# Performance work log

Measured on AMD Instinct MI355X. Metric: run time of the kernel, lower is better.

Reference implementation:

```python
import jax, jax.numpy as jnp
import numpy as np

B, S, D = 2, 2048, 1024
FFN = 4096
E, TOPK = 4, 2
H, WIN = 8, 128
EPS = 1e-6


def rmsnorm(x, w):
    rms = jax.lax.rsqrt(jnp.mean(x * x, axis=-1, keepdims=True) + EPS)
    return x * rms * w


def linear_scan(x, a):
    """h_t = a_t * h_{t-1} + x_t along axis=1, via associative scan."""
    def comb(c1, c2):
        a1, x1 = c1
        a2, x2 = c2
        return (a1 * a2, a2 * x1 + x2)
    _, h = jax.lax.associative_scan(comb, (a, x), axis=1)
    return h


def mingru_expert(xn, Wg, bg, Wv, bv, Wd, bd):
    g = xn @ Wg + bg
    v = xn @ Wv + bv
    d = xn @ Wd + bd
    x_scan = jax.nn.sigmoid(g) * jnp.tanh(v)
    a = 0.001 + 0.998 * jax.nn.sigmoid(d)
    return linear_scan(x_scan, a)


def setup_inputs() -> dict:
    key = jax.random.key(0)
    ks = jax.random.split(key, 16)
    sc = 0.02
    return {
        "x": jax.random.normal(ks[0], (B, S, D), jnp.float32),
        "rms_mix_w": jnp.ones((D,), jnp.float32),
        "gate_w": jax.random.normal(ks[1], (D, E), jnp.float32) * sc,
        "Wg": jax.random.normal(ks[2], (E, D, D), jnp.float32) * sc,
        "bg": jnp.zeros((E, D), jnp.float32),
        "Wv": jax.random.normal(ks[3], (E, D, D), jnp.float32) * sc,
        "bv": jnp.zeros((E, D), jnp.float32),
        "Wd": jax.random.normal(ks[4], (E, D, D), jnp.float32) * sc,
        "bd": jnp.ones((E, D), jnp.float32),  # decay_bias_init = 1.0
        "rms_attn_w": jnp.ones((D,), jnp.float32),
        "w_qkv": jax.random.normal(ks[5], (D, 3 * D), jnp.float32) * sc,
        "w_attn_out": jax.random.normal(ks[6], (D, D), jnp.float32) * sc,
        "rms_ffn_w": jnp.ones((D,), jnp.float32),
        "w_ffn_gate": jax.random.normal(ks[7], (D, FFN), jnp.float32) * sc,
        "w_ffn_up": jax.random.normal(ks[8], (D, FFN), jnp.float32) * sc,
        "w_ffn_out": jax.random.normal(ks[9], (FFN, D), jnp.float32) * sc,
    }


def reference(x, rms_mix_w, gate_w, Wg, bg, Wv, bv, Wd, bd,
              rms_attn_w, w_qkv, w_attn_out,
              rms_ffn_w, w_ffn_gate, w_ffn_up, w_ffn_out):
    # --- MoE-MinGRU mixer -------------------------------------------------
    xn = rmsnorm(x, rms_mix_w)
    gate_logits = xn @ gate_w                         # [B,S,E]
    top_vals, top_idx = jax.lax.top_k(gate_logits, TOPK)
    weights = jax.nn.softmax(top_vals, axis=-1)       # [B,S,K]
    expert_outs = jax.vmap(mingru_expert, in_axes=(None, 0, 0, 0, 0, 0, 0))(
        xn, Wg, bg, Wv, bv, Wd, bd)                   # [E,B,S,D]
    expert_outs = jnp.moveaxis(expert_outs, 0, 2)     # [B,S,E,D]
    gathered = jnp.take_along_axis(expert_outs, top_idx[..., None], axis=2)  # [B,S,K,D]
    mix = jnp.sum(weights[..., None] * gathered, axis=2)
    x = x + mix

    # --- Sliding-window causal attention ----------------------------------
    xn = rmsnorm(x, rms_attn_w)
    dh = D // H
    qkv = (xn @ w_qkv).reshape(B, S, 3, H, dh)
    q, k, v = qkv[:, :, 0], qkv[:, :, 1], qkv[:, :, 2]  # [B,S,H,dh]
    scores = jnp.einsum("bqhd,bkhd->bhqk", q, k) / jnp.sqrt(jnp.float32(dh))
    i = jnp.arange(S)[:, None]
    j = jnp.arange(S)[None, :]
    allowed = (j <= i) & (j > i - WIN)
    scores = jnp.where(allowed, scores, -jnp.inf)
    attn = jax.nn.softmax(scores, axis=-1)
    ao = jnp.einsum("bhqk,bkhd->bqhd", attn, v).reshape(B, S, D)
    x = x + ao @ w_attn_out

    # --- SwiGLU FFN --------------------------------------------------------
    xn = rmsnorm(x, rms_ffn_w)
    ffn = (jax.nn.silu(xn @ w_ffn_gate) * (xn @ w_ffn_up)) @ w_ffn_out
    return x + ffn
```

## Files before the change

kernel.cpp:

```cpp
#include <hip/hip_runtime.h>
#include <hip/hip_bf16.h>
#include <math.h>

constexpr int kB   = 2;
constexpr int kS   = 2048;
constexpr int kD   = 1024;
constexpr int kFFN = 4096;
constexpr int kM   = kB * kS;
constexpr int kH   = 8;
constexpr int kDH  = 128;
constexpr int kNC  = 64;
constexpr int kT   = kS / kNC;
constexpr int kNE  = 12288;

typedef unsigned short u16;
typedef __attribute__((ext_vector_type(8))) short short8;
typedef __attribute__((ext_vector_type(4))) float f32x4;

__device__ __forceinline__ float sigf(float x) { return 1.0f / (1.0f + __expf(-x)); }
__device__ __forceinline__ float bu2f(u16 u) { return __uint_as_float(((unsigned)u) << 16); }
__device__ __forceinline__ u16 f2bu(float f) {
    __hip_bfloat16 h = __float2bfloat16(f);
    return reinterpret_cast<u16&>(h);
}
__device__ __forceinline__ void async16(const void* g, void* l) {
    __builtin_amdgcn_global_load_lds((const __attribute__((address_space(1))) void*)g,
                                     (__attribute__((address_space(3))) void*)l, 16, 0, 0);
}
__device__ __forceinline__ int xcd_swz(int orig, int nwg) {
    const int xcd = orig & 7;
    const int q8 = nwg >> 3, r8 = nwg & 7;
    return (xcd < r8 ? xcd * (q8 + 1) : r8 * (q8 + 1) + (xcd - r8) * q8) + (orig >> 3);
}

__global__ __launch_bounds__(256) void rmsnorm_k(const float* __restrict__ x,
                                                 const float* __restrict__ w,
                                                 u16* __restrict__ o)
{
    __shared__ float red[4];
    const int row = blockIdx.x;
    const int t = threadIdx.x;
    float4 v = ((const float4*)(x + (size_t)row * kD))[t];
    float ss = v.x*v.x + v.y*v.y + v.z*v.z + v.w*v.w;
    #pragma unroll
    for (int m = 32; m; m >>= 1) ss += __shfl_xor(ss, m);
    if ((t & 63) == 0) red[t >> 6] = ss;
    __syncthreads();
    float tot = red[0] + red[1] + red[2] + red[3];
    float r = rsqrtf(tot * (1.0f / (float)kD) + 1e-6f);
    float4 wv = ((const float4*)w)[t];
    ushort4 u;
    u.x = f2bu(v.x * r * wv.x); u.y = f2bu(v.y * r * wv.y);
    u.z = f2bu(v.z * r * wv.z); u.w = f2bu(v.w * r * wv.w);
    ((ushort4*)(o + (size_t)row * kD))[t] = u;
}

__global__ __launch_bounds__(64) void routing_k(const float* __restrict__ x,
                                                const float* __restrict__ wmix,
                                                const float* __restrict__ gw,
                                                float* __restrict__ wts,
                                                int* __restrict__ idx)
{
    const int row = blockIdx.x;
    const int lane = threadIdx.x;
    const float* xr = x + (size_t)row * kD;
    float ss = 0.0f;
    for (int d = lane; d < kD; d += 64) { float v = xr[d]; ss = fmaf(v, v, ss); }
    #pragma unroll
    for (int m = 32; m; m >>= 1) ss += __shfl_xor(ss, m);
    float r = rsqrtf(ss * (1.0f / (float)kD) + 1e-6f);

    float a0 = 0, a1 = 0, a2 = 0, a3 = 0;
    for (int d = lane; d < kD; d += 64) {
        float xv = xr[d] * wmix[d];
        float4 g = ((const float4*)gw)[d];
        a0 = fmaf(xv, g.x, a0);
        a1 = fmaf(xv, g.y, a1);
        a2 = fmaf(xv, g.z, a2);
        a3 = fmaf(xv, g.w, a3);
    }
    #pragma unroll
    for (int m = 32; m; m >>= 1) {
        a0 += __shfl_xor(a0, m);
        a1 += __shfl_xor(a1, m);
        a2 += __shfl_xor(a2, m);
        a3 += __shfl_xor(a3, m);
    }
    if (lane == 0) {
        float a[4] = {a0, a1, a2, a3};
        int i0 = 0; float v0 = a[0];
        #pragma unroll
        for (int e = 1; e < 4; ++e) if (a[e] > v0) { v0 = a[e]; i0 = e; }
        int i1 = -1; float v1 = -INFINITY;
        #pragma unroll
        for (int e = 0; e < 4; ++e) if (e != i0 && a[e] > v1) { v1 = a[e]; i1 = e; }
        float e1 = __expf(r * (v1 - v0));
        float dn = 1.0f + e1;
        wts[row * 2 + 0] = 1.0f / dn;
        wts[row * 2 + 1] = e1 / dn;
        idx[row * 2 + 0] = i0;
        idx[row * 2 + 1] = i1;
    }
}

__global__ __launch_bounds__(256) void transp_k(const float* __restrict__ src,
                                                u16* __restrict__ dst,
                                                int rows, int cols,
                                                size_t sstride, size_t dstride)
{
    __shared__ float t[32][33];
    const float* s = src + blockIdx.z * sstride;
    u16* d = dst + blockIdx.z * dstride;
    const int c0 = blockIdx.x * 32, r0 = blockIdx.y * 32;
    const int tc = threadIdx.x & 31, tr4 = (threadIdx.x >> 5) * 4;
    #pragma unroll
    for (int i = 0; i < 4; ++i)
        t[tr4 + i][tc] = s[(size_t)(r0 + tr4 + i) * cols + c0 + tc];
    __syncthreads();
    #pragma unroll
    for (int i = 0; i < 4; ++i) {
        int cc = tr4 + i;
        d[(size_t)(c0 + cc) * rows + r0 + tc] = f2bu(t[tc][cc]);
    }
}

__global__ __launch_bounds__(256) void biaspack_k(const float* __restrict__ bg,
                                                  const float* __restrict__ bv,
                                                  const float* __restrict__ bd,
                                                  float* __restrict__ pb)
{
    int e = blockIdx.y;
    int r = blockIdx.x * 256 + threadIdx.x;
    const float* src = (r < 1024) ? bg : (r < 2048) ? bv : bd;
    pb[e * 3072 + r] = src[e * 1024 + (r & 1023)];
}

template<bool BIAS, bool SILU, bool MUL>
__global__ __launch_bounds__(512, 2) void gemmA_k(
    const u16* __restrict__ A, const u16* __restrict__ BT,
    const float* __restrict__ bias, const u16* __restrict__ mulsrc,
    u16* __restrict__ Cout, int N, int K)
{
    __shared__ __align__(16) u16 lds[2][32768];
    const int tid = threadIdx.x;
    const int l = tid & 63;
    const int w = tid >> 6;
    const int wr = w >> 2, wc = w & 3;
    const int fr = l & 15, g = l >> 4;

    const int gx = gridDim.x;
    const int wg = xcd_swz(blockIdx.y * gx + blockIdx.x, gx * gridDim.y);
    const int bm = (wg / gx) * 256, bn = (wg % gx) * 256;

    const int srow = l >> 3;
    const int scol = (l & 7) ^ srow;
    const u16* gA = A  + (size_t)(bm + srow) * K + scol * 8;
    const u16* gB = BT + (size_t)(bn + srow) * K + scol * 8;

    auto STAGE = [&](int kt, int sb) {
        u16* dst = lds[sb] + l * 8;
        const int k0 = kt * 64;
        #pragma unroll
        for (int i = 0; i < 4; ++i) {
            int chunk = w * 4 + i;
            async16(gA + (size_t)chunk * 8 * K + k0, dst + chunk * 512);
            async16(gB + (size_t)chunk * 8 * K + k0, dst + 16384 + chunk * 512);
        }
    };

    f32x4 acc[8][4];
    #pragma unroll
    for (int m = 0; m < 8; ++m)
        #pragma unroll
        for (int n = 0; n < 4; ++n) acc[m][n] = (f32x4){0.f, 0.f, 0.f, 0.f};

    STAGE(0, 0);
    __syncthreads();
    const int nt = K >> 6;
    for (int t = 0; t < nt; ++t) {
        const int cb = t & 1;
        if (t + 1 < nt) STAGE(t + 1, cb ^ 1);
        const u16* bA = lds[cb];
        const u16* bB = lds[cb] + 16384;
        #pragma unroll
        for (int ks = 0; ks < 2; ++ks) {
            const int xo = ((ks * 4 + g) ^ (fr & 7)) * 8;
            short8 b[4];
            #pragma unroll
            for (int n = 0; n < 4; ++n)
                b[n] = *(const short8*)(bB + (wc * 64 + n * 16 + fr) * 64 + xo);
            #pragma unroll
            for (int m = 0; m < 8; ++m) {
                short8 a = *(const short8*)(bA + (wr * 128 + m * 16 + fr) * 64 + xo);
                #pragma unroll
                for (int n = 0; n < 4; ++n)
                    acc[m][n] = __builtin_amdgcn_mfma_f32_16x16x32_bf16(a, b[n], acc[m][n], 0, 0, 0);
            }
        }
        __syncthreads();
    }

    const int orow0 = bm + wr * 128 + g * 4;
    const int ocol0 = bn + wc * 64 + fr;
    float bi[4];
    if constexpr (BIAS) {
        #pragma unroll
        for (int n = 0; n < 4; ++n) bi[n] = bias[ocol0 + n * 16];
    }
    #pragma unroll
    for (int m = 0; m < 8; ++m) {
        #pragma unroll
        for (int r = 0; r < 4; ++r) {
            const size_t ro = (size_t)(orow0 + m * 16 + r) * N;
            #pragma unroll
            for (int n = 0; n < 4; ++n) {
                const size_t off = ro + ocol0 + n * 16;
                float v = acc[m][n][r];
                if constexpr (BIAS) v += bi[n];
                if constexpr (SILU) v = v * sigf(v);
                if constexpr (MUL)  v *= bu2f(mulsrc[off]);
                Cout[off] = f2bu(v);
            }
        }
    }
}

__global__ __launch_bounds__(256, 2) void gemmO_k(
    const u16* __restrict__ A, const u16* __restrict__ BT,
    const float* __restrict__ res, float* __restrict__ Cout,
    int N, int K)
{
    __shared__ __align__(16) u16 lds[3][20480];
    const int tid = threadIdx.x;
    const int l = tid & 63;
    const int w = tid >> 6;
    const int fr = l & 15, g = l >> 4;

    const int gx = gridDim.x;
    const int wg = xcd_swz(blockIdx.y * gx + blockIdx.x, gx * gridDim.y);
    const int bm = (wg / gx) * 256, bn = (wg % gx) * 64;

    const int srow = l >> 3;
    const int scol = (l & 7) ^ srow;
    const u16* gA = A  + (size_t)(bm + srow) * K + scol * 8;
    const u16* gB = BT + (size_t)(bn + srow) * K + scol * 8;

    auto STAGE = [&](int kt, int sb) {
        u16* dst = lds[sb] + l * 8;
        const int k0 = kt * 64;
        #pragma unroll
        for (int i = 0; i < 8; ++i) {
            int chunk = w * 8 + i;
            async16(gA + (size_t)chunk * 8 * K + k0, dst + chunk * 512);
        }
        #pragma unroll
        for (int i = 0; i < 2; ++i) {
            int chunk = w * 2 + i;
            async16(gB + (size_t)chunk * 8 * K + k0, dst + 16384 + chunk * 512);
        }
    };

    f32x4 acc[4][4];
    #pragma unroll
    for (int m = 0; m < 4; ++m)
        #pragma unroll
        for (int n = 0; n < 4; ++n) acc[m][n] = (f32x4){0.f, 0.f, 0.f, 0.f};

    STAGE(0, 0);
    STAGE(1, 1);
    const int nt = K >> 6;
    int cs = 0;
    for (int t = 0; t < nt; ++t) {
        if (t + 1 < nt) asm volatile("s_waitcnt vmcnt(10)" ::: "memory");
        else            asm volatile("s_waitcnt vmcnt(0)" ::: "memory");
        __builtin_amdgcn_s_barrier();
        __builtin_amdgcn_sched_barrier(0);
        if (t + 2 < nt) {
            int ns = cs + 2; if (ns >= 3) ns -= 3;
            STAGE(t + 2, ns);
        }
        const u16* bA = lds[cs];
        const u16* bB = lds[cs] + 16384;
        #pragma unroll
        for (int ks = 0; ks < 2; ++ks) {
            const int xo = ((ks * 4 + g) ^ (fr & 7)) * 8;
            short8 a[4], b[4];
            #pragma unroll
            for (int m = 0; m < 4; ++m)
                a[m] = *(const short8*)(bA + (w * 64 + m * 16 + fr) * 64 + xo);
            #pragma unroll
            for (int n = 0; n < 4; ++n)
                b[n] = *(const short8*)(bB + (n * 16 + fr) * 64 + xo);
            #pragma unroll
            for (int m = 0; m < 4; ++m)
                #pragma unroll
                for (int n = 0; n < 4; ++n)
                    acc[m][n] = __builtin_amdgcn_mfma_f32_16x16x32_bf16(a[m], b[n], acc[m][n], 0, 0, 0);
        }
        cs = (cs == 2) ? 0 : cs + 1;
    }

    const int orow0 = bm + w * 64 + g * 4;
    const int ocol0 = bn + fr;
    #pragma unroll
    for (int m = 0; m < 4; ++m) {
        #pragma unroll
        for (int r = 0; r < 4; ++r) {
            const size_t ro = (size_t)(orow0 + m * 16 + r) * N;
            #pragma unroll
            for (int n = 0; n < 4; ++n) {
                const size_t off = ro + ocol0 + n * 16;
                Cout[off] = acc[m][n][r] + res[off];
            }
        }
    }
}

__global__ __launch_bounds__(256) void scan1_k(const u16* __restrict__ gvdall,
                                               float* __restrict__ sumA,
                                               float* __restrict__ sumX)
{
    const int e = blockIdx.y;
    int i = blockIdx.x * 256 + threadIdx.x;
    int d = i & (kD - 1);
    int c = (i >> 10) & (kNC - 1);
    int b = i >> 16;
    const u16* gvd = gvdall + e * 3072;
    size_t base = ((size_t)b * kS + c * kT) * kNE + d;
    float A = 1.0f, X = 0.0f;
    for (int t = 0; t < kT; ++t) {
        size_t ix = base + (size_t)t * kNE;
        float xs = sigf(bu2f(gvd[ix])) * tanhf(bu2f(gvd[ix + 1024]));
        float a  = 0.001f + 0.998f * sigf(bu2f(gvd[ix + 2048]));
        A *= a;
        X = fmaf(a, X, xs);
    }
    size_t si = ((size_t)(e * kNC + c) * kB + b) * kD + d;
    sumA[si] = A;
    sumX[si] = X;
}

__global__ __launch_bounds__(256) void scan2_k(const float* __restrict__ sumA,
                                               const float* __restrict__ sumX,
                                               float* __restrict__ carry)
{
    const int e = blockIdx.y;
    int bd = blockIdx.x * 256 + threadIdx.x;
    float h = 0.0f;
    for (int c = 0; c < kNC; ++c) {
        size_t si = ((size_t)(e * kNC + c)) * (kB * kD) + bd;
        carry[si] = h;
        h = fmaf(sumA[si], h, sumX[si]);
    }
}

__global__ __launch_bounds__(256) void scan3_k(const u16* __restrict__ gvdall,
                                               const float* __restrict__ carry,
                                               const int* __restrict__ tidx,
                                               u16* __restrict__ slot0,
                                               u16* __restrict__ slot1)
{
    const int e = blockIdx.y;
    int i = blockIdx.x * 256 + threadIdx.x;
    int d = i & (kD - 1);
    int c = (i >> 10) & (kNC - 1);
    int b = i >> 16;
    const u16* gvd = gvdall + e * 3072;
    size_t base = ((size_t)b * kS + c * kT) * kNE + d;
    float h = carry[((size_t)(e * kNC + c) * kB + b) * kD + d];
    const int tok0 = b * kS + c * kT;
    for (int t = 0; t < kT; ++t) {
        size_t ix = base + (size_t)t * kNE;
        float xs = sigf(bu2f(gvd[ix])) * tanhf(bu2f(gvd[ix + 1024]));
        float a  = 0.001f + 0.998f * sigf(bu2f(gvd[ix + 2048]));
        h = fmaf(a, h, xs);
        const int tok = tok0 + t;
        const size_t o = (size_t)tok * kD + d;
        if (e == tidx[tok * 2])          slot0[o] = f2bu(h);
        else if (e == tidx[tok * 2 + 1]) slot1[o] = f2bu(h);
    }
}

__global__ __launch_bounds__(256) void mix_k(const float* __restrict__ x,
                                             const u16* __restrict__ slot0,
                                             const u16* __restrict__ slot1,
                                             const float* __restrict__ wts,
                                             float* __restrict__ xo)
{
    size_t i = (size_t)blockIdx.x * 256 + threadIdx.x;
    int m = (int)(i >> 8);
    float w0 = wts[m * 2 + 0], w1 = wts[m * 2 + 1];
    float4 xv = ((const float4*)x)[i];
    ushort4 h0 = ((const ushort4*)slot0)[i];
    ushort4 h1 = ((const ushort4*)slot1)[i];
    float4 o;
    o.x = xv.x + w0 * bu2f(h0.x) + w1 * bu2f(h1.x);
    o.y = xv.y + w0 * bu2f(h0.y) + w1 * bu2f(h1.y);
    o.z = xv.z + w0 * bu2f(h0.z) + w1 * bu2f(h1.z);
    o.w = xv.w + w0 * bu2f(h0.w) + w1 * bu2f(h1.w);
    ((float4*)xo)[i] = o;
}

__global__ __launch_bounds__(256) void transpV_k(const u16* __restrict__ qkvb,
                                                 u16* __restrict__ vT)
{
    __shared__ u16 t[64][68];
    const int tid = threadIdx.x;
    const int s0 = blockIdx.x * 64;
    const int d0 = blockIdx.y * 64;
    const int bh = blockIdx.z;
    const int bb = bh >> 3, hh = bh & 7;
    const u16* src = qkvb + (size_t)(bb * kS + s0) * 3072 + 2048 + hh * kDH + d0;
    for (int idx = tid; idx < 64 * 16; idx += 256) {
        int sl = idx >> 4, c4 = (idx & 15) * 4;
        *(ushort4*)&t[sl][c4] = *(const ushort4*)(src + (size_t)sl * 3072 + c4);
    }
    __syncthreads();
    u16* dst = vT + ((size_t)bh * kDH + d0) * kS + s0;
    for (int idx = tid; idx < 64 * 16; idx += 256) {
        int dl = idx >> 4, s4 = (idx & 15) * 4;
        ushort4 v;
        v.x = t[s4 + 0][dl]; v.y = t[s4 + 1][dl];
        v.z = t[s4 + 2][dl]; v.w = t[s4 + 3][dl];
        *(ushort4*)(dst + (size_t)dl * kS + s4) = v;
    }
}

__global__ __launch_bounds__(256) void attn_mfma_k(const u16* __restrict__ qkvb,
                                                   const u16* __restrict__ vT,
                                                   u16* __restrict__ aob)
{
    __shared__ __align__(16) u16 KV[26112];
    __shared__ __align__(16) u16 P[4 * 16 * 200];

    const int tid = threadIdx.x;
    const int lane = tid & 63;
    const int w = tid >> 6;
    const int fr = lane & 15, g = lane >> 4;
    const int q0 = blockIdx.x * 64;
    const int hh = blockIdx.y;
    const int bb = blockIdx.z;
    const int kbase = q0 - 128;
    const float scale = 0.08838834764831845f;

    const u16* qkv_b = qkvb + (size_t)bb * kS * 3072 + hh * kDH;

    for (int idx = tid; idx < 192 * 16; idx += 256) {
        int k = idx >> 4, c = idx & 15;
        int kg = kbase + k; if (kg < 0) kg = 0;
        short8 v = *(const short8*)(qkv_b + (size_t)kg * 3072 + 1024 + c * 8);
        *(short8*)(&KV[k * 136 + c * 8]) = v;
    }
    short8 qf[4];
    {
        const u16* qrow = qkv_b + (size_t)(q0 + w * 16 + fr) * 3072 + g * 8;
        #pragma unroll
        for (int s = 0; s < 4; ++s) qf[s] = *(const short8*)(qrow + s * 32);
    }
    __syncthreads();

    f32x4 sacc[12];
    #pragma unroll
    for (int f = 0; f < 12; ++f) sacc[f] = (f32x4){0.f, 0.f, 0.f, 0.f};
    #pragma unroll
    for (int s = 0; s < 4; ++s) {
        #pragma unroll
        for (int f = 0; f < 12; ++f) {
            short8 bfr = *(const short8*)(&KV[(f * 16 + fr) * 136 + s * 32 + g * 8]);
            sacc[f] = __builtin_amdgcn_mfma_f32_16x16x32_bf16(qf[s], bfr, sacc[f], 0, 0, 0);
        }
    }

    float p[12][4];
    #pragma unroll
    for (int r = 0; r < 4; ++r) {
        const int ql = w * 16 + g * 4 + r;
        int kmin = 128 - q0; if (kmin < ql + 1) kmin = ql + 1;
        const int kmax = ql + 128;
        float mx = -1e30f;
        #pragma unroll
        for (int f = 0; f < 12; ++f) {
            int kl = f * 16 + fr;
            float sv = (kl >= kmin && kl <= kmax) ? sacc[f][r] * scale : -1e30f;
            p[f][r] = sv;
            mx = fmaxf(mx, sv);
        }
        mx = fmaxf(mx, __shfl_xor(mx, 1));
        mx = fmaxf(mx, __shfl_xor(mx, 2));
        mx = fmaxf(mx, __shfl_xor(mx, 4));
        mx = fmaxf(mx, __shfl_xor(mx, 8));
        float l = 0.f;
        #pragma unroll
        for (int f = 0; f < 12; ++f) { float e = __expf(p[f][r] - mx); p[f][r] = e; l += e; }
        l += __shfl_xor(l, 1);
        l += __shfl_xor(l, 2);
        l += __shfl_xor(l, 4);
        l += __shfl_xor(l, 8);
        float linv = 1.0f / l;
        #pragma unroll
        for (int f = 0; f < 12; ++f) p[f][r] *= linv;
    }

    {
        u16* pw = &P[(w * 16) * 200];
        #pragma unroll
        for (int r = 0; r < 4; ++r)
            #pragma unroll
            for (int f = 0; f < 12; ++f)
                pw[(g * 4 + r) * 200 + f * 16 + fr] = f2bu(p[f][r]);
    }
    __syncthreads();

    {
        const u16* vrow = vT + (size_t)(bb * kH + hh) * kDH * kS;
        for (int idx = tid; idx < 128 * 25; idx += 256) {
            int d = idx / 25, c = idx % 25;
            if (c < 24) {
                int s0k = kbase + c * 8;
                short8 v;
                if (s0k < 0) v = (short8){0, 0, 0, 0, 0, 0, 0, 0};
                else v = *(const short8*)(vrow + (size_t)d * kS + s0k);
                *(short8*)(&KV[d * 200 + c * 8]) = v;
            }
        }
    }
    __syncthreads();

    f32x4 oacc[8];
    #pragma unroll
    for (int f = 0; f < 8; ++f) oacc[f] = (f32x4){0.f, 0.f, 0.f, 0.f};
    const u16* pr = &P[(w * 16 + fr) * 200 + g * 8];
    #pragma unroll
    for (int s = 0; s < 6; ++s) {
        short8 afr = *(const short8*)(pr + s * 32);
        #pragma unroll
        for (int f = 0; f < 8; ++f) {
            short8 bfr = *(const short8*)(&KV[(f * 16 + fr) * 200 + s * 32 + g * 8]);
            oacc[f] = __builtin_amdgcn_mfma_f32_16x16x32_bf16(afr, bfr, oacc[f], 0, 0, 0);
        }
    }
    u16* orow = aob + ((size_t)(bb * kS + q0 + w * 16 + g * 4) * kD) + hh * kDH + fr;
    #pragma unroll
    for (int r = 0; r < 4; ++r)
        #pragma unroll
        for (int f = 0; f < 8; ++f)
            orow[(size_t)r * kD + f * 16] = f2bu(oacc[f][r]);
}

extern "C" void kernel_launch(void* const* d_in, const int* in_sizes, int n_in,
                              void* d_out, int out_size, void* d_ws, size_t ws_size,
                              hipStream_t stream)
{
    (void)in_sizes; (void)n_in; (void)out_size; (void)ws_size;

    const float* x          = (const float*)d_in[0];
    const float* rms_mix    = (const float*)d_in[1];
    const float* gate_w     = (const float*)d_in[2];
    const float* Wg         = (const float*)d_in[3];
    const float* bg         = (const float*)d_in[4];
    const float* Wv         = (const float*)d_in[5];
    const float* bv         = (const float*)d_in[6];
    const float* Wd         = (const float*)d_in[7];
    const float* bd         = (const float*)d_in[8];
    const float* rms_attn   = (const float*)d_in[9];
    const float* w_qkv      = (const float*)d_in[10];
    const float* w_attn_out = (const float*)d_in[11];
    const float* rms_ffn    = (const float*)d_in[12];
    const float* w_ffn_gate = (const float*)d_in[13];
    const float* w_ffn_up   = (const float*)d_in[14];
    const float* w_ffn_out  = (const float*)d_in[15];
    float* out = (float*)d_out;

    const size_t MD = (size_t)kM * kD;
    const size_t M1 = 1024ull * 1024;
    char* p = (char*)d_ws;
    auto take = [&](size_t n) { char* r = p; p += (n + 255) & ~(size_t)255; return r; };

    u16*   xnb    = (u16*)take(MD * 2);
    u16*   gvdall = (u16*)take((size_t)kM * kNE * 2);
    u16*   qkvb   = gvdall;
    u16*   hidA   = gvdall;
    u16*   hidB   = gvdall + (size_t)kM * kFFN;
    u16*   ehb    = (u16*)take(4 * MD * 2);
    u16*   slot0  = ehb;
    u16*   slot1  = ehb + MD;
    u16*   aob    = ehb;
    u16*   vTb    = ehb + MD;
    u16*   wbuf   = (u16*)take(12ull * M1 * 2);
    float* pbias  = (float*)take((size_t)kNE * 4);
    float* sumA   = (float*)take(4ull * kNC * kB * kD * 4);
    float* sumX   = (float*)take(4ull * kNC * kB * kD * 4);
    float* carry  = (float*)take(4ull * kNC * kB * kD * 4);
    float* wts    = (float*)take((size_t)2 * kM * 4);
    int*   tidx   = (int*)take((size_t)2 * kM * 4);

    const dim3 blk(256);

    transp_k<<<dim3(32, 32, 4), blk, 0, stream>>>(Wg, wbuf, 1024, 1024,
                                                  (size_t)kD * kD, 3 * M1);
    transp_k<<<dim3(32, 32, 4), blk, 0, stream>>>(Wv, wbuf + M1, 1024, 1024,
                                                  (size_t)kD * kD, 3 * M1);
    transp_k<<<dim3(32, 32, 4), blk, 0, stream>>>(Wd, wbuf + 2 * M1, 1024, 1024,
                                                  (size_t)kD * kD, 3 * M1);
    biaspack_k<<<dim3(12, 4), blk, 0, stream>>>(bg, bv, bd, pbias);

    rmsnorm_k<<<kM, blk, 0, stream>>>(x, rms_mix, xnb);
    routing_k<<<kM, dim3(64), 0, stream>>>(x, rms_mix, gate_w, wts, tidx);

    gemmA_k<true, false, false><<<dim3(kNE / 256, kM / 256), dim3(512), 0, stream>>>(
        xnb, wbuf, pbias, nullptr, gvdall, kNE, 1024);
    const int scan_blocks = kB * kD * kNC / 256;
    scan1_k<<<dim3(scan_blocks, 4), blk, 0, stream>>>(gvdall, sumA, sumX);
    scan2_k<<<dim3(kB * kD / 256, 4), blk, 0, stream>>>(sumA, sumX, carry);
    scan3_k<<<dim3(scan_blocks, 4), blk, 0, stream>>>(gvdall, carry, tidx, slot0, slot1);

    mix_k<<<(int)(MD / 1024), blk, 0, stream>>>(x, slot0, slot1, wts, out);

    rmsnorm_k<<<kM, blk, 0, stream>>>(out, rms_attn, xnb);
    transp_k<<<dim3(96, 32, 1), blk, 0, stream>>>(w_qkv, wbuf, 1024, 3072, 0, 0);
    gemmA_k<false, false, false><<<dim3(3072 / 256, kM / 256), dim3(512), 0, stream>>>(
        xnb, wbuf, nullptr, nullptr, qkvb, 3072, 1024);
    transpV_k<<<dim3(kS / 64, 2, kB * kH), blk, 0, stream>>>(qkvb, vTb);
    attn_mfma_k<<<dim3(kS / 64, kH, kB), blk, 0, stream>>>(qkvb, vTb, aob);
    transp_k<<<dim3(32, 32, 1), blk, 0, stream>>>(w_attn_out, wbuf + 3 * M1, 1024, 1024, 0, 0);
    gemmO_k<<<dim3(1024 / 64, kM / 256), blk, 0, stream>>>(
        aob, wbuf + 3 * M1, out, out, 1024, 1024);

    rmsnorm_k<<<kM, blk, 0, stream>>>(out, rms_ffn, xnb);
    transp_k<<<dim3(128, 32, 1), blk, 0, stream>>>(w_ffn_gate, wbuf + 4 * M1, 1024, 4096, 0, 0);
    transp_k<<<dim3(128, 32, 1), blk, 0, stream>>>(w_ffn_up, wbuf + 8 * M1, 1024, 4096, 0, 0);
    transp_k<<<dim3(32, 128, 1), blk, 0, stream>>>(w_ffn_out, wbuf, 4096, 1024, 0, 0);
    gemmA_k<false, true, false><<<dim3(kFFN / 256, kM / 256), dim3(512), 0, stream>>>(
        xnb, wbuf + 4 * M1, nullptr, nullptr, hidA, kFFN, 1024);
    gemmA_k<false, false, true><<<dim3(kFFN / 256, kM / 256), dim3(512), 0, stream>>>(
        xnb, wbuf + 8 * M1, nullptr, hidA, hidB, kFFN, 1024);
    gemmO_k<<<dim3(1024 / 64, kM / 256), blk, 0, stream>>>(
        hidB, wbuf, out, out, 1024, 4096);
}
```

Baseline: 479.1 us.

## Rework output GEMM to 512-thread double-buffered tiles; nontemporal expert stores

The output-projection GEMM now uses 8 warps in a 4x2 arrangement, each computing a 64x32 sub-tile, with a simpler double-buffered LDS pipeline synchronized by __syncthreads instead of a triple-buffered vmcnt-based pipeline. This aims to raise parallelism per block and cut per-thread accumulator registers, at the cost of a shallower prefetch depth and full barriers each iteration. The large expert-projection GEMM also writes its bf16 output with nontemporal stores, to reduce cache pollution from a buffer that is streamed once by the scan kernels.

Measured after the change: 484.5 us (median of 3 runs). No clear change (+1.1%).

```diff
diff --git a/kernel.cpp b/kernel.cpp
--- a/kernel.cpp
+++ b/kernel.cpp
@@ -135,7 +135,7 @@
     pb[e * 3072 + r] = src[e * 1024 + (r & 1023)];
 }
 
-template<bool BIAS, bool SILU, bool MUL>
+template<bool BIAS, bool SILU, bool MUL, bool NT>
 __global__ __launch_bounds__(512, 2) void gemmA_k(
     const u16* __restrict__ A, const u16* __restrict__ BT,
     const float* __restrict__ bias, const u16* __restrict__ mulsrc,
@@ -219,21 +219,23 @@
                 if constexpr (BIAS) v += bi[n];
                 if constexpr (SILU) v = v * sigf(v);
                 if constexpr (MUL)  v *= bu2f(mulsrc[off]);
-                Cout[off] = f2bu(v);
+                if constexpr (NT) __builtin_nontemporal_store((short)f2bu(v), (short*)(Cout + off));
+                else              Cout[off] = f2bu(v);
             }
         }
     }
 }
 
-__global__ __launch_bounds__(256, 2) void gemmO_k(
+__global__ __launch_bounds__(512, 2) void gemmO_k(
     const u16* __restrict__ A, const u16* __restrict__ BT,
     const float* __restrict__ res, float* __restrict__ Cout,
     int N, int K)
 {
-    __shared__ __align__(16) u16 lds[3][20480];
+    __shared__ __align__(16) u16 lds[2][20480];
     const int tid = threadIdx.x;
     const int l = tid & 63;
     const int w = tid >> 6;
+    const int wr = w >> 1, wc = w & 1;
     const int fr = l & 15, g = l >> 4;
 
     const int gx = gridDim.x;
@@ -249,66 +251,55 @@
         u16* dst = lds[sb] + l * 8;
         const int k0 = kt * 64;
         #pragma unroll
-        for (int i = 0; i < 8; ++i) {
-            int chunk = w * 8 + i;
+        for (int i = 0; i < 4; ++i) {
+            int chunk = w * 4 + i;
             async16(gA + (size_t)chunk * 8 * K + k0, dst + chunk * 512);
         }
-        #pragma unroll
-        for (int i = 0; i < 2; ++i) {
-            int chunk = w * 2 + i;
-            async16(gB + (size_t)chunk * 8 * K + k0, dst + 16384 + chunk * 512);
-        }
+        async16(gB + (size_t)w * 8 * K + k0, dst + 16384 + w * 512);
     };
 
-    f32x4 acc[4][4];
+    f32x4 acc[4][2];
     #pragma unroll
     for (int m = 0; m < 4; ++m)
         #pragma unroll
-        for (int n = 0; n < 4; ++n) acc[m][n] = (f32x4){0.f, 0.f, 0.f, 0.f};
+        for (int n = 0; n < 2; ++n) acc[m][n] = (f32x4){0.f, 0.f, 0.f, 0.f};
 
     STAGE(0, 0);
-    STAGE(1, 1);
+    __syncthreads();
     const int nt = K >> 6;
-    int cs = 0;
     for (int t = 0; t < nt; ++t) {
-        if (t + 1 < nt) asm volatile("s_waitcnt vmcnt(10)" ::: "memory");
-        else            asm volatile("s_waitcnt vmcnt(0)" ::: "memory");
-        __builtin_amdgcn_s_barrier();
-        __builtin_amdgcn_sched_barrier(0);
-        if (t + 2 < nt) {
-            int ns = cs + 2; if (ns >= 3) ns -= 3;
-            STAGE(t + 2, ns);
-        }
-        const u16* bA = lds[cs];
-        const u16* bB = lds[cs] + 16384;
+        const int cb = t & 1;
+        if (t + 1 < nt) STAGE(t + 1, cb ^ 1);
+        const u16* bA = lds[cb];
+        const u16* bB = lds[cb] + 16384;
         #pragma unroll
         for (int ks = 0; ks < 2; ++ks) {
             const int xo = ((ks * 4 + g) ^ (fr & 7)) * 8;
-            short8 a[4], b[4];
+            short8 a[4], b[2];
             #pragma unroll
             for (int m = 0; m < 4; ++m)
-                a[m] = *(const short8*)(bA + (w * 64 + m * 16 + fr) * 64 + xo);
-            #pragma unroll
-            for (int n = 0; n < 4; ++n)
-                b[n] = *(const short8*)(bB + (n * 16 + fr) * 64 + xo);
+                a[m] = *(const short8*)(bA + (wr * 64 + m * 16 + fr) * 64 + xo);
+            #pragma unroll
+            for (int n = 0; n < 2; ++n)
+                b[n] = *(const short8*)(bB + (wc * 32 + n * 16 + fr) * 64 + xo);
             #pragma unroll
             for (int m = 0; m < 4; ++m)
                 #pragma unroll
-                for (int n = 0; n < 4; ++n)
+                for (int n = 0; n < 2; ++n)
                     acc[m][n] = __builtin_amdgcn_mfma_f32_16x16x32_bf16(a[m], b[n], acc[m][n], 0, 0, 0);
         }
-        cs = (cs == 2) ? 0 : cs + 1;
-    }
-
-    const int orow0 = bm + w * 64 + g * 4;
-    const int ocol0 = bn + fr;
+        __syncthreads();
+    }
+
+    const int orow0 = bm + wr * 64 + g * 4;
+    const int ocol0 = bn + wc * 32 + fr;
     #pragma unroll
     for (int m = 0; m < 4; ++m) {
         #pragma unroll
         for (int r = 0; r < 4; ++r) {
             const size_t ro = (size_t)(orow0 + m * 16 + r) * N;
             #pragma unroll
-            for (int n = 0; n < 4; ++n) {
+            for (int n = 0; n < 2; ++n) {
                 const size_t off = ro + ocol0 + n * 16;
                 Cout[off] = acc[m][n][r] + res[off];
             }
@@ -607,7 +598,7 @@
     rmsnorm_k<<<kM, blk, 0, stream>>>(x, rms_mix, xnb);
     routing_k<<<kM, dim3(64), 0, stream>>>(x, rms_mix, gate_w, wts, tidx);
 
-    gemmA_k<true, false, false><<<dim3(kNE / 256, kM / 256), dim3(512), 0, stream>>>(
+    gemmA_k<true, false, false, true><<<dim3(kNE / 256, kM / 256), dim3(512), 0, stream>>>(
         xnb, wbuf, pbias, nullptr, gvdall, kNE, 1024);
     const int scan_blocks = kB * kD * kNC / 256;
     scan1_k<<<dim3(scan_blocks, 4), blk, 0, stream>>>(gvdall, sumA, sumX);
@@ -618,22 +609,22 @@
 
     rmsnorm_k<<<kM, blk, 0, stream>>>(out, rms_attn, xnb);
     transp_k<<<dim3(96, 32, 1), blk, 0, stream>>>(w_qkv, wbuf, 1024, 3072, 0, 0);
-    gemmA_k<false, false, false><<<dim3(3072 / 256, kM / 256), dim3(512), 0, stream>>>(
+    gemmA_k<false, false, false, false><<<dim3(3072 / 256, kM / 256), dim3(512), 0, stream>>>(
         xnb, wbuf, nullptr, nullptr, qkvb, 3072, 1024);
     transpV_k<<<dim3(kS / 64, 2, kB * kH), blk, 0, stream>>>(qkvb, vTb);
     attn_mfma_k<<<dim3(kS / 64, kH, kB), blk, 0, stream>>>(qkvb, vTb, aob);
     transp_k<<<dim3(32, 32, 1), blk, 0, stream>>>(w_attn_out, wbuf + 3 * M1, 1024, 1024, 0, 0);
-    gemmO_k<<<dim3(1024 / 64, kM / 256), blk, 0, stream>>>(
+    gemmO_k<<<dim3(1024 / 64, kM / 256), dim3(512), 0, stream>>>(
         aob, wbuf + 3 * M1, out, out, 1024, 1024);
 
     rmsnorm_k<<<kM, blk, 0, stream>>>(out, rms_ffn, xnb);
     transp_k<<<dim3(128, 32, 1), blk, 0, stream>>>(w_ffn_gate, wbuf + 4 * M1, 1024, 4096, 0, 0);
     transp_k<<<dim3(128, 32, 1), blk, 0, stream>>>(w_ffn_up, wbuf + 8 * M1, 1024, 4096, 0, 0);
     transp_k<<<dim3(32, 128, 1), blk, 0, stream>>>(w_ffn_out, wbuf, 4096, 1024, 0, 0);
-    gemmA_k<false, true, false><<<dim3(kFFN / 256, kM / 256), dim3(512), 0, stream>>>(
+    gemmA_k<false, true, false, false><<<dim3(kFFN / 256, kM / 256), dim3(512), 0, stream>>>(
         xnb, wbuf + 4 * M1, nullptr, nullptr, hidA, kFFN, 1024);
-    gemmA_k<false, false, true><<<dim3(kFFN / 256, kM / 256), dim3(512), 0, stream>>>(
+    gemmA_k<false, false, true, false><<<dim3(kFFN / 256, kM / 256), dim3(512), 0, stream>>>(
         xnb, wbuf + 8 * M1, nullptr, hidA, hidB, kFFN, 1024);
-    gemmO_k<<<dim3(1024 / 64, kM / 256), blk, 0, stream>>>(
+    gemmO_k<<<dim3(1024 / 64, kM / 256), dim3(512), 0, stream>>>(
         hidB, wbuf, out, out, 1024, 4096);
 }
```
